# Kernel optimization log

Hardware: AMD Instinct MI355X
Metric: run time of the kernel (lower is better)

Reference implementation:

```python
import jax, jax.numpy as jnp
import numpy as np

H = 1024          # hid_dim
SEQ = 149         # input tokens (cls makes 150)
B = 128           # batch
WIN = 20          # local attention band half-width (hard-coded in module)


def _pe_table(n, d):
    # ConstantPE with period=1: position = 2*pi*arange(n)
    pos = 2.0 * np.pi * np.arange(n, dtype=np.float64)[:, None]
    div = np.exp(np.arange(0, d, 2, dtype=np.float64) * (-np.log(10000.0) / d))
    pe = np.zeros((n, d), dtype=np.float32)
    pe[:, 0::2] = np.sin(pos * div)
    pe[:, 1::2] = np.cos(pos * div)
    return jnp.asarray(pe)


def _band_mask(n, w=WIN):
    # True where attention is DISALLOWED (matches src_mask == 1)
    r = np.arange(n)[:, None]
    c = np.arange(n)[None, :]
    allowed = (c >= np.maximum(r - w, 0)) & (c < r + w)
    allowed[0, :] = True  # cls row attends everywhere
    return jnp.asarray(~allowed)


def _layer_norm(x, g, b, eps=1e-5):
    m = jnp.mean(x, axis=-1, keepdims=True)
    v = jnp.var(x, axis=-1, keepdims=True)
    return (x - m) * jax.lax.rsqrt(v + eps) * g + b


def setup_inputs() -> dict:
    key = jax.random.key(0)
    ks = jax.random.split(key, 8)
    s = 0.02
    return {
        "z": jax.random.normal(ks[0], (SEQ, B, H), jnp.float32),
        "cls_token": jax.random.normal(ks[1], (1, H), jnp.float32),
        "ln_g": jnp.ones((H,), jnp.float32),
        "ln_b": jnp.zeros((H,), jnp.float32),
        "w_qkv": jax.random.normal(ks[2], (H, 3 * H), jnp.float32) * s,
        "b_qkv": jnp.zeros((3 * H,), jnp.float32),
        "w_o": jax.random.normal(ks[3], (H, H), jnp.float32) * s,
        "b_o": jnp.zeros((H,), jnp.float32),
        "w_m1": jax.random.normal(ks[4], (H, H), jnp.float32) * s,
        "b_m1": jnp.zeros((H,), jnp.float32),
        "w_m2": jax.random.normal(ks[5], (H, H), jnp.float32) * s,
        "b_m2": jnp.zeros((H,), jnp.float32),
    }


def reference(z, cls_token, ln_g, ln_b, w_qkv, b_qkv, w_o, b_o, w_m1, b_m1, w_m2, b_m2):
    S1 = z.shape[0] + 1  # tokens incl. cls
    pe = _pe_table(S1, H)          # (S1, H)
    neg_mask = _band_mask(S1)      # (S1, S1) bool, True = masked

    x = jnp.swapaxes(z, 0, 1)                                   # (B, S, H)
    cls = jnp.broadcast_to(cls_token[None], (x.shape[0], 1, H))  # (B, 1, H)
    x = jnp.concatenate([cls, x], axis=1)                        # (B, S1, H)
    x = _layer_norm(x + pe[None], ln_g, ln_b)

    qkv = x @ w_qkv + b_qkv
    q, k, v = jnp.split(qkv, 3, axis=-1)

    attn = jnp.einsum("bqh,bkh->bqk", q, k) / jnp.sqrt(jnp.float32(H))
    attn = jnp.where(neg_mask[None], jnp.float32(-1e10), attn)
    attn = jax.nn.softmax(attn, axis=-1)

    sa = jnp.einsum("bqk,bkh->bqh", attn, v) @ w_o + b_o
    zsa = _layer_norm(x + sa, ln_g, ln_b)

    mlp = jax.nn.gelu(zsa @ w_m1 + b_m1, approximate=False) @ w_m2 + b_m2
    out = zsa + mlp
    return jnp.swapaxes(out, 0, 1)  # (S1, B, H)
```

## Files before the change

kernel.cpp:

```cpp
#include <hip/hip_runtime.h>
#include <math.h>

#define HD 1024
#define S1 150
#define BATCH 128
#define MTOK (S1 * BATCH)
#define WIN 20
#define QKVLD (3 * HD)

typedef unsigned short bf16_t;
typedef short s16x8 __attribute__((ext_vector_type(8)));
typedef float f32x4 __attribute__((ext_vector_type(4)));

__device__ __forceinline__ float bf2f(unsigned int u16) {
  return __uint_as_float(u16 << 16);
}
__device__ __forceinline__ unsigned short f2bf(float f) {
  unsigned int u = __float_as_uint(f);
  u += 0x7fff + ((u >> 16) & 1);
  return (unsigned short)(u >> 16);
}

__device__ __forceinline__ float wave_sum(float v) {
#pragma unroll
  for (int o = 32; o; o >>= 1) v += __shfl_down(v, o, 64);
  return v;
}

__device__ __forceinline__ void gload_lds16(const bf16_t* g, bf16_t* l) {
  __builtin_amdgcn_global_load_lds(
      (const __attribute__((address_space(1))) unsigned int*)(unsigned long long)(const void*)g,
      (__attribute__((address_space(3))) unsigned int*)(unsigned int)(unsigned long long)(void*)l,
      16, 0, 0);
}

__global__ __launch_bounds__(256) void transpose_all_kernel(
    const float* __restrict__ w_qkv, bf16_t* __restrict__ wt_qkv,
    const float* __restrict__ w_o, bf16_t* __restrict__ wt_o,
    const float* __restrict__ w_m1, bf16_t* __restrict__ wt_m1,
    const float* __restrict__ w_m2, bf16_t* __restrict__ wt_m2) {
  int g = blockIdx.x;
  const float* W;
  bf16_t* WT;
  int N, bx, by;
  if (g < 3072) {
    W = w_qkv; WT = wt_qkv; N = 3072;
    bx = g % 96; by = g / 96;
  } else {
    int r = g - 3072;
    int which = r >> 10, l = r & 1023;
    bx = l & 31; by = l >> 5; N = 1024;
    W = (which == 0) ? w_o : (which == 1) ? w_m1 : w_m2;
    WT = (which == 0) ? wt_o : (which == 1) ? wt_m1 : wt_m2;
  }
  __shared__ float t[32][33];
  int n0 = bx * 32, k0 = by * 32;
  int tx = threadIdx.x, ty = threadIdx.y;
#pragma unroll
  for (int i = 0; i < 4; i++)
    t[ty + i * 8][tx] = W[(size_t)(k0 + ty + i * 8) * N + n0 + tx];
  __syncthreads();
#pragma unroll
  for (int i = 0; i < 4; i++)
    WT[(size_t)(n0 + ty + i * 8) * 1024 + k0 + tx] = f2bf(t[tx][ty + i * 8]);
}

__global__ void pe_kernel(float* __restrict__ pe) {
  int s = blockIdx.x;
  double pos = 6.283185307179586476925286766559 * (double)s;
  for (int p = threadIdx.x; p < HD / 2; p += blockDim.x) {
    double dv = exp((double)(2 * p) * (-9.210340371976184 / (double)HD));
    double a = pos * dv;
    pe[s * HD + 2 * p] = (float)sin(a);
    pe[s * HD + 2 * p + 1] = (float)cos(a);
  }
}

__global__ __launch_bounds__(256) void build_x_kernel(
    const float* __restrict__ z, const float* __restrict__ cls,
    const float* __restrict__ pe, const float* __restrict__ g,
    const float* __restrict__ be, bf16_t* __restrict__ x) {
  int t = blockIdx.x;
  int b = t / S1, s = t % S1;
  const float* src = (s == 0) ? cls : (z + ((size_t)(s - 1) * BATCH + b) * HD);
  const float* pr = pe + (size_t)s * HD;
  int tid = threadIdx.x;
  float vals[4];
  float sum = 0.f, sq = 0.f;
#pragma unroll
  for (int i = 0; i < 4; i++) {
    int h = tid + i * 256;
    float v = src[h] + pr[h];
    vals[i] = v;
    sum += v;
    sq += v * v;
  }
  __shared__ float shs[4], shq[4];
  __shared__ float sm, sr;
  sum = wave_sum(sum);
  sq = wave_sum(sq);
  int wave = tid >> 6, lane = tid & 63;
  if (!lane) { shs[wave] = sum; shq[wave] = sq; }
  __syncthreads();
  if (!tid) {
    float S = shs[0] + shs[1] + shs[2] + shs[3];
    float Q = shq[0] + shq[1] + shq[2] + shq[3];
    float mean = S * (1.f / HD);
    float var = Q * (1.f / HD) - mean * mean;
    sm = mean;
    sr = rsqrtf(var + 1e-5f);
  }
  __syncthreads();
  float mean = sm, rstd = sr;
  bf16_t* xr = x + (size_t)t * HD;
#pragma unroll
  for (int i = 0; i < 4; i++) {
    int h = tid + i * 256;
    xr[h] = f2bf((vals[i] - mean) * rstd * g[h] + be[h]);
  }
}

__global__ __launch_bounds__(256) void ln_residual_kernel(
    const bf16_t* __restrict__ a, const bf16_t* __restrict__ r,
    const float* __restrict__ g, const float* __restrict__ be,
    bf16_t* __restrict__ out) {
  int t = blockIdx.x;
  int tid = threadIdx.x;
  const bf16_t* ar = a + (size_t)t * QKVLD;
  const bf16_t* rr = r + (size_t)t * HD;
  float vals[4];
  float sum = 0.f, sq = 0.f;
#pragma unroll
  for (int i = 0; i < 4; i++) {
    int h = tid + i * 256;
    float v = bf2f(ar[h]) + bf2f(rr[h]);
    vals[i] = v;
    sum += v;
    sq += v * v;
  }
  __shared__ float shs[4], shq[4];
  __shared__ float sm, sr;
  sum = wave_sum(sum);
  sq = wave_sum(sq);
  int wave = tid >> 6, lane = tid & 63;
  if (!lane) { shs[wave] = sum; shq[wave] = sq; }
  __syncthreads();
  if (!tid) {
    float S = shs[0] + shs[1] + shs[2] + shs[3];
    float Q = shq[0] + shq[1] + shq[2] + shq[3];
    float mean = S * (1.f / HD);
    float var = Q * (1.f / HD) - mean * mean;
    sm = mean;
    sr = rsqrtf(var + 1e-5f);
  }
  __syncthreads();
  float mean = sm, rstd = sr;
  bf16_t* outp = out + (size_t)t * QKVLD;
#pragma unroll
  for (int i = 0; i < 4; i++) {
    int h = tid + i * 256;
    outp[h] = f2bf((vals[i] - mean) * rstd * g[h] + be[h]);
  }
}

template <int EPI>
__global__ __launch_bounds__(256) void mfma_gemm_kernel(
    const bf16_t* __restrict__ A, int lda, const bf16_t* __restrict__ WT,
    const float* __restrict__ bias, bf16_t* __restrict__ C, int ldc,
    const bf16_t* __restrict__ res, float* __restrict__ outf) {
  constexpr int K = 1024;
  __shared__ bf16_t As[2 * 128 * 32];
  __shared__ bf16_t Bs[2 * 128 * 32];
  int tid = threadIdx.x;
  int w = tid >> 6, lane = tid & 63;
  int wm = w >> 1, wn = w & 1;
  int m0 = blockIdx.y * 128, n0 = blockIdx.x * 128;

  int srow = lane >> 2;
  int scol = ((lane & 3) ^ ((lane >> 3) & 3)) * 8;
  const bf16_t* gA0 = A + (size_t)(m0 + w * 32 + srow) * lda + scol;
  const bf16_t* gA1 = gA0 + (size_t)16 * lda;
  const bf16_t* gB0 = WT + (size_t)(n0 + w * 32 + srow) * K + scol;
  const bf16_t* gB1 = gB0 + (size_t)16 * K;
  bf16_t* lA0 = As + (w * 32) * 32;
  bf16_t* lA1 = As + (w * 32 + 16) * 32;
  bf16_t* lB0 = Bs + (w * 32) * 32;
  bf16_t* lB1 = Bs + (w * 32 + 16) * 32;

  int frow = lane & 15;
  int slot = (lane >> 4) ^ ((frow >> 1) & 3);
  int aoff[4], boff[4];
#pragma unroll
  for (int t = 0; t < 4; t++) {
    aoff[t] = (wm * 64 + t * 16 + frow) * 32 + slot * 8;
    boff[t] = (wn * 64 + t * 16 + frow) * 32 + slot * 8;
  }

  f32x4 acc[4][4] = {};

  for (int k0 = 0; k0 < K; k0 += 64) {
    gload_lds16(gA0, lA0);
    gload_lds16(gA1, lA1);
    gload_lds16(gB0, lB0);
    gload_lds16(gB1, lB1);
    gload_lds16(gA0 + 32, lA0 + 4096);
    gload_lds16(gA1 + 32, lA1 + 4096);
    gload_lds16(gB0 + 32, lB0 + 4096);
    gload_lds16(gB1 + 32, lB1 + 4096);
    gA0 += 64; gA1 += 64; gB0 += 64; gB1 += 64;
    __syncthreads();
#pragma unroll
    for (int p = 0; p < 2; p++) {
      s16x8 af[4], bf[4];
#pragma unroll
      for (int t = 0; t < 4; t++) {
        af[t] = *(const s16x8*)(As + p * 4096 + aoff[t]);
        bf[t] = *(const s16x8*)(Bs + p * 4096 + boff[t]);
      }
#pragma unroll
      for (int i = 0; i < 4; i++)
#pragma unroll
        for (int j = 0; j < 4; j++)
          acc[i][j] = __builtin_amdgcn_mfma_f32_16x16x32_bf16(af[i], bf[j], acc[i][j], 0, 0, 0);
    }
    __syncthreads();
  }

  int erow = (lane >> 4) * 4, ecol = lane & 15;
#pragma unroll
  for (int j = 0; j < 4; j++) {
    int n = n0 + wn * 64 + j * 16 + ecol;
    float bb = bias[n];
#pragma unroll
    for (int i = 0; i < 4; i++) {
      int mb = m0 + wm * 64 + i * 16 + erow;
#pragma unroll
      for (int r = 0; r < 4; r++) {
        int m = mb + r;
        float v = acc[i][j][r] + bb;
        if (EPI == 1) v = 0.5f * v * (1.f + erff(v * 0.7071067811865476f));
        if (EPI == 2) {
          int b = m / S1, s = m % S1;
          v += bf2f(res[(size_t)m * QKVLD + n]);
          outf[((size_t)s * BATCH + b) * HD + n] = v;
        } else {
          C[(size_t)m * ldc + n] = f2bf(v);
        }
      }
    }
  }
}

__global__ __launch_bounds__(256) void attn_tile_kernel(bf16_t* __restrict__ qkv) {
  int g = blockIdx.x;
  int xcd = g & 7, tt0 = g >> 3;
  int qt = tt0 % 5, b = xcd + 8 * (tt0 / 5);
  int q0 = qt * 32;

  int lo_col = (qt == 0) ? 0 : (q0 - 20);
  int hi_col = (qt == 0) ? 150 : ((q0 + 51 < 150) ? q0 + 51 : 150);
  int ct0 = lo_col >> 5;
  int cth = (hi_col + 31) >> 5;
  int NCT = cth - ct0;
  int W = NCT * 32;
  int NSUB = NCT * 2;
  int NT = 2 * NSUB;
  int T = NT >> 2;

  __shared__ bf16_t Qs[2 * 32 * 32];
  __shared__ bf16_t Ks[2 * 160 * 32];
  __shared__ float S[32][164];

  int tid = threadIdx.x;
  int w = tid >> 6, lane = tid & 63;

  const bf16_t* kvbase = qkv + (size_t)b * S1 * QKVLD;

  int sr = lane >> 2;
  int scol = ((lane & 3) ^ ((lane >> 3) & 3)) * 8;
  int frow = lane & 15;
  int fslot = (((lane >> 4) ^ ((frow >> 1) & 3))) * 8;

  f32x4 acc[5] = {};

  int U1 = 2 + NSUB;

  for (int k0 = 0; k0 < 1024; k0 += 64) {
    for (int uu = w; uu < 2 * U1; uu += 4) {
      int p = (uu >= U1) ? 1 : 0;
      int ur = uu - p * U1;
      int col = k0 + p * 32 + scol;
      if (ur < 2) {
        int qrow = q0 + ur * 16 + sr;
        if (qrow > 149) qrow = 149;
        gload_lds16(kvbase + (size_t)qrow * QKVLD + col,
                    Qs + p * 1024 + (ur * 16) * 32);
      } else {
        int cr0 = (ur - 2) * 16;
        int cg = ct0 * 32 + cr0 + sr;
        if (cg > 149) cg = 149;
        gload_lds16(kvbase + (size_t)cg * QKVLD + HD + col,
                    Ks + p * 5120 + cr0 * 32);
      }
    }
    __syncthreads();
    s16x8 af0[2], af1[2];
#pragma unroll
    for (int p = 0; p < 2; p++) {
      af0[p] = *(const s16x8*)(Qs + p * 1024 + (0 * 16 + frow) * 32 + fslot);
      af1[p] = *(const s16x8*)(Qs + p * 1024 + (1 * 16 + frow) * 32 + fslot);
    }
#pragma unroll
    for (int t = 0; t < 5; t++) {
      if (t < T) {
        int tidt = w + t * 4;
        int qs = (tidt >= NSUB) ? 1 : 0;
        int cs = tidt - qs * NSUB;
#pragma unroll
        for (int p = 0; p < 2; p++) {
          s16x8 bf = *(const s16x8*)(Ks + p * 5120 + (cs * 16 + frow) * 32 + fslot);
          s16x8 a = qs ? af1[p] : af0[p];
          acc[t] = __builtin_amdgcn_mfma_f32_16x16x32_bf16(a, bf, acc[t], 0, 0, 0);
        }
      }
    }
    __syncthreads();
  }

  int erow = (lane >> 4) * 4, ecol = lane & 15;
#pragma unroll
  for (int t = 0; t < 5; t++) {
    if (t < T) {
      int tidt = w + t * 4;
      int qs = (tidt >= NSUB) ? 1 : 0;
      int cs = tidt - qs * NSUB;
#pragma unroll
      for (int r = 0; r < 4; r++) {
        int qrel = qs * 16 + erow + r;
        int crel = cs * 16 + ecol;
        int qg = q0 + qrel, cg = ct0 * 32 + crel;
        bool ok = (qg < 150) && (cg < 150) &&
                  ((qg == 0) || (cg >= qg - WIN && cg < qg + WIN));
        S[qrel][crel] = ok ? acc[t][r] * 0.03125f : -1e30f;
      }
    }
  }
  __syncthreads();

  {
    int q = tid >> 3, j = tid & 7;
    float m = -1e30f;
    for (int c = j; c < W; c += 8) m = fmaxf(m, S[q][c]);
#pragma unroll
    for (int o = 1; o < 8; o <<= 1) m = fmaxf(m, __shfl_xor(m, o, 64));
    float s = 0.f;
    for (int c = j; c < W; c += 8) {
      float e = __expf(S[q][c] - m);
      S[q][c] = e;
      s += e;
    }
#pragma unroll
    for (int o = 1; o < 8; o <<= 1) s += __shfl_xor(s, o, 64);
    float inv = 1.f / s;
    for (int c = j; c < W; c += 8) S[q][c] *= inv;
  }
  __syncthreads();

  int qg0 = q0 + 8 * w;
  if (qg0 < 150) {
    int lo = (qt == 0 && w == 0) ? 0 : ((qg0 - WIN > 0) ? qg0 - WIN : 0);
    int hi = (qt == 0 && w == 0) ? 150 : ((qg0 + 27 < 150) ? qg0 + 27 : 150);
    int c0base = ct0 * 32;
#pragma unroll
    for (int hp = 0; hp < 2; hp++) {
      int hb = hp * 512 + lane * 8;
      float a[8][8];
#pragma unroll
      for (int qi = 0; qi < 8; qi++)
#pragma unroll
        for (int e = 0; e < 8; e++) a[qi][e] = 0.f;
      const bf16_t* vb = kvbase + 2 * HD + hb;
      for (int c = lo; c < hi; ++c) {
        uint4 vv = *(const uint4*)(vb + (size_t)c * QKVLD);
        float vf[8];
        vf[0] = __uint_as_float(vv.x << 16);
        vf[1] = __uint_as_float(vv.x & 0xffff0000u);
        vf[2] = __uint_as_float(vv.y << 16);
        vf[3] = __uint_as_float(vv.y & 0xffff0000u);
        vf[4] = __uint_as_float(vv.z << 16);
        vf[5] = __uint_as_float(vv.z & 0xffff0000u);
        vf[6] = __uint_as_float(vv.w << 16);
        vf[7] = __uint_as_float(vv.w & 0xffff0000u);
        int crel = c - c0base;
#pragma unroll
        for (int qi = 0; qi < 8; qi++) {
          float p = S[8 * w + qi][crel];
#pragma unroll
          for (int e = 0; e < 8; e++) a[qi][e] += p * vf[e];
        }
      }
#pragma unroll
      for (int qi = 0; qi < 8; qi++) {
        int qg = qg0 + qi;
        if (qg < 150) {
          uint4 pk;
          pk.x = (unsigned int)f2bf(a[qi][0]) | ((unsigned int)f2bf(a[qi][1]) << 16);
          pk.y = (unsigned int)f2bf(a[qi][2]) | ((unsigned int)f2bf(a[qi][3]) << 16);
          pk.z = (unsigned int)f2bf(a[qi][4]) | ((unsigned int)f2bf(a[qi][5]) << 16);
          pk.w = (unsigned int)f2bf(a[qi][6]) | ((unsigned int)f2bf(a[qi][7]) << 16);
          *(uint4*)(qkv + ((size_t)b * S1 + qg) * QKVLD + hb) = pk;
        }
      }
    }
  }
}

extern "C" void kernel_launch(void* const* d_in, const int* in_sizes, int n_in,
                              void* d_out, int out_size, void* d_ws, size_t ws_size,
                              hipStream_t stream) {
  (void)in_sizes; (void)n_in; (void)out_size; (void)ws_size;
  const float* z = (const float*)d_in[0];
  const float* cls = (const float*)d_in[1];
  const float* ln_g = (const float*)d_in[2];
  const float* ln_b = (const float*)d_in[3];
  const float* w_qkv = (const float*)d_in[4];
  const float* b_qkv = (const float*)d_in[5];
  const float* w_o = (const float*)d_in[6];
  const float* b_o = (const float*)d_in[7];
  const float* w_m1 = (const float*)d_in[8];
  const float* b_m1 = (const float*)d_in[9];
  const float* w_m2 = (const float*)d_in[10];
  const float* b_m2 = (const float*)d_in[11];

  char* wsb = (char*)d_ws;
  bf16_t* wt_m2 = (bf16_t*)wsb;
  float* pe = (float*)(wsb + 2097152);
  bf16_t* qkv = (bf16_t*)(wsb + 2097152 + 614400);

  char* outb = (char*)d_out;
  bf16_t* x = (bf16_t*)outb;
  bf16_t* wt_qkv = (bf16_t*)(outb + 39321600);
  bf16_t* wt_o = (bf16_t*)(outb + 45613056);
  bf16_t* wt_m1 = (bf16_t*)(outb + 47710208);

  bf16_t* av = qkv;
  bf16_t* sa = qkv + HD;
  bf16_t* zsa = qkv + 2 * HD;
  bf16_t* h1 = qkv;
  float* out = (float*)d_out;

  transpose_all_kernel<<<6144, dim3(32, 8), 0, stream>>>(
      w_qkv, wt_qkv, w_o, wt_o, w_m1, wt_m1, w_m2, wt_m2);
  pe_kernel<<<S1, 256, 0, stream>>>(pe);
  build_x_kernel<<<MTOK, 256, 0, stream>>>(z, cls, pe, ln_g, ln_b, x);
  mfma_gemm_kernel<0><<<dim3(24, 150), 256, 0, stream>>>(
      x, HD, wt_qkv, b_qkv, qkv, QKVLD, nullptr, nullptr);
  attn_tile_kernel<<<640, 256, 0, stream>>>(qkv);
  mfma_gemm_kernel<0><<<dim3(8, 150), 256, 0, stream>>>(
      av, QKVLD, wt_o, b_o, sa, QKVLD, nullptr, nullptr);
  ln_residual_kernel<<<MTOK, 256, 0, stream>>>(sa, x, ln_g, ln_b, zsa);
  mfma_gemm_kernel<1><<<dim3(8, 150), 256, 0, stream>>>(
      zsa, QKVLD, wt_m1, b_m1, h1, QKVLD, nullptr, nullptr);
  mfma_gemm_kernel<2><<<dim3(8, 150), 256, 0, stream>>>(
      h1, QKVLD, wt_m2, b_m2, nullptr, 0, zsa, out);
}
```

Measured before the change: 695.5 us.

## Swizzle GEMM workgroups across XCDs and stage bf16 epilogue through LDS

Workgroup indices in the MFMA GEMM are remapped so consecutive blocks on the same XCD cover neighbouring output tiles, which should improve L2 reuse of A and weight tiles. For the non-residual epilogues, the bf16 results are first written into the shared-memory buffer that the mainloop already used. They are then stored with 16-byte row-contiguous writes instead of scattered 2-byte stores. This adds an extra barrier and LDS traffic, and the swizzle assumes the workgroup count divides evenly by 8.

```diff
diff --git a/kernel.cpp b/kernel.cpp
--- a/kernel.cpp
+++ b/kernel.cpp
@@ -169,12 +169,18 @@
     const float* __restrict__ bias, bf16_t* __restrict__ C, int ldc,
     const bf16_t* __restrict__ res, float* __restrict__ outf) {
   constexpr int K = 1024;
-  __shared__ bf16_t As[2 * 128 * 32];
-  __shared__ bf16_t Bs[2 * 128 * 32];
+  __shared__ bf16_t SMEM[16384];
+  bf16_t* As = SMEM;
+  bf16_t* Bs = SMEM + 8192;
   int tid = threadIdx.x;
   int w = tid >> 6, lane = tid & 63;
   int wm = w >> 1, wn = w & 1;
-  int m0 = blockIdx.y * 128, n0 = blockIdx.x * 128;
+
+  int nwg = gridDim.x * gridDim.y;
+  int g = blockIdx.y * gridDim.x + blockIdx.x;
+  int swz = (g & 7) * (nwg >> 3) + (g >> 3);
+  int bx = swz % gridDim.x, by = swz / gridDim.x;
+  int m0 = by * 128, n0 = bx * 128;
 
   int srow = lane >> 2;
   int scol = ((lane & 3) ^ ((lane >> 3) & 3)) * 8;
@@ -227,26 +233,46 @@
   }
 
   int erow = (lane >> 4) * 4, ecol = lane & 15;
-#pragma unroll
-  for (int j = 0; j < 4; j++) {
-    int n = n0 + wn * 64 + j * 16 + ecol;
-    float bb = bias[n];
-#pragma unroll
-    for (int i = 0; i < 4; i++) {
-      int mb = m0 + wm * 64 + i * 16 + erow;
-#pragma unroll
-      for (int r = 0; r < 4; r++) {
-        int m = mb + r;
-        float v = acc[i][j][r] + bb;
-        if (EPI == 1) v = 0.5f * v * (1.f + erff(v * 0.7071067811865476f));
-        if (EPI == 2) {
+  if (EPI == 2) {
+#pragma unroll
+    for (int j = 0; j < 4; j++) {
+      int n = n0 + wn * 64 + j * 16 + ecol;
+      float bb = bias[n];
+#pragma unroll
+      for (int i = 0; i < 4; i++) {
+        int mb = m0 + wm * 64 + i * 16 + erow;
+#pragma unroll
+        for (int r = 0; r < 4; r++) {
+          int m = mb + r;
           int b = m / S1, s = m % S1;
-          v += bf2f(res[(size_t)m * QKVLD + n]);
+          float v = acc[i][j][r] + bb + bf2f(res[(size_t)m * QKVLD + n]);
           outf[((size_t)s * BATCH + b) * HD + n] = v;
-        } else {
-          C[(size_t)m * ldc + n] = f2bf(v);
         }
       }
+    }
+  } else {
+#pragma unroll
+    for (int j = 0; j < 4; j++) {
+      int cn = wn * 64 + j * 16 + ecol;
+      float bb = bias[n0 + cn];
+#pragma unroll
+      for (int i = 0; i < 4; i++) {
+        int cmb = wm * 64 + i * 16 + erow;
+#pragma unroll
+        for (int r = 0; r < 4; r++) {
+          float v = acc[i][j][r] + bb;
+          if (EPI == 1) v = 0.5f * v * (1.f + erff(v * 0.7071067811865476f));
+          SMEM[(cmb + r) * 128 + cn] = f2bf(v);
+        }
+      }
+    }
+    __syncthreads();
+    int rr = tid >> 4, cb = (tid & 15) * 8;
+#pragma unroll
+    for (int p = 0; p < 8; p++) {
+      int row = p * 16 + rr;
+      *(uint4*)(C + (size_t)(m0 + row) * ldc + n0 + cb) =
+          *(const uint4*)(SMEM + row * 128 + cb);
     }
   }
 }
```

After: 674.9 us. 3.0% less time.
